# Performance work log

Measured on AMD Instinct MI355X. Metric: run time of the kernel, lower is better.

Reference implementation:

```python
import jax, jax.numpy as jnp
import numpy as np

C = 256
DK = C // 8  # query/key channels


def setup_inputs() -> dict:
    key = jax.random.key(0)
    ks = jax.random.split(key, 7)
    B, W, H = 4, 64, 64
    x = jax.random.normal(ks[0], (B, C, W, H), dtype=jnp.float32)
    s_in = 1.0 / np.sqrt(C)
    Wq = jax.random.normal(ks[1], (DK, C), dtype=jnp.float32) * s_in
    bq = jnp.zeros((DK,), dtype=jnp.float32)
    Wk = jax.random.normal(ks[2], (DK, C), dtype=jnp.float32) * s_in
    bk = jnp.zeros((DK,), dtype=jnp.float32)
    Wv = jax.random.normal(ks[3], (C, C), dtype=jnp.float32) * s_in
    bv = jnp.zeros((C,), dtype=jnp.float32)
    return {"x": x, "Wq": Wq, "bq": bq, "Wk": Wk, "bk": bk, "Wv": Wv, "bv": bv}


def reference(x, Wq, bq, Wk, bk, Wv, bv):
    B, Cc, W, H = x.shape
    N = W * H
    xf = x.reshape(B, Cc, N)  # (B, C, N) flattened spatial
    # 1x1 convs == channel matmuls
    q = jnp.einsum('dc,bcn->bnd', Wq, xf) + bq  # (B, N, DK)
    k = jnp.einsum('dc,bcn->bdn', Wk, xf) + bk[None, :, None]  # (B, DK, N)
    v = jnp.einsum('oc,bcn->bon', Wv, xf) + bv[None, :, None]  # (B, C, N)
    energy = jnp.einsum('bnd,bdm->bnm', q, k) / jnp.sqrt(jnp.float32(q.shape[-1]))
    attn = jax.nn.softmax(energy, axis=-1)  # (B, N, N)
    out = jnp.einsum('bcn,bmn->bcm', v, attn)  # v @ attn^T
    return out.reshape(B, Cc, W, H) + x
```

## Files before the change

kernel.cpp:

```cpp
#include <hip/hip_runtime.h>
#include <hip/hip_bf16.h>
#include <math.h>

#define BB 4
#define CC 256
#define DKK 32
#define NN 4096
#define QSCALE 0.2550181864060454f

typedef __attribute__((ext_vector_type(8))) __bf16 bf16x8;
typedef __attribute__((ext_vector_type(4))) __bf16 bf16x4;
typedef __attribute__((ext_vector_type(4))) float f32x4;

#define XST 260
#define SCRST 65

__global__ __launch_bounds__(256) void qkv_kernel(
    const float* __restrict__ x,
    const float* __restrict__ Wq, const float* __restrict__ bq,
    const float* __restrict__ Wk, const float* __restrict__ bk,
    const float* __restrict__ Wv, const float* __restrict__ bv,
    __bf16* __restrict__ qws, __bf16* __restrict__ kws, __bf16* __restrict__ vws)
{
    __shared__ __align__(16) unsigned char smem[50688];
    __bf16* xsT  = (__bf16*)smem;
    float*  xs32 = (float*)(smem + 33280);
    float*  scr  = (float*)(smem + 33280);

    const int tid = threadIdx.x;
    const int w   = tid >> 6;
    const int l   = tid & 63;
    const int l15 = l & 15;
    const int lq  = l >> 4;
    const int n0  = blockIdx.x * 64;
    const int b   = blockIdx.y;

    for (int cr = 0; cr < 4; cr++) {
#pragma unroll
        for (int p = 0; p < 4; p++) {
            int cc = p * 16 + (tid >> 4);
            int nf = (tid & 15) * 4;
            float4 v = *(const float4*)&x[((size_t)(b * CC + cr * 64 + cc)) * NN + n0 + nf];
            *(float4*)&xs32[cc * 68 + nf] = v;
        }
        __syncthreads();
        {
            int n = tid >> 2, cs = (tid & 3) * 16;
            bf16x4 t0, t1, t2, t3;
#pragma unroll
            for (int j = 0; j < 4; j++) {
                t0[j] = (__bf16)xs32[(cs + j)      * 68 + n];
                t1[j] = (__bf16)xs32[(cs + 4 + j)  * 68 + n];
                t2[j] = (__bf16)xs32[(cs + 8 + j)  * 68 + n];
                t3[j] = (__bf16)xs32[(cs + 12 + j) * 68 + n];
            }
            *(bf16x4*)&xsT[n * XST + cr * 64 + cs]      = t0;
            *(bf16x4*)&xsT[n * XST + cr * 64 + cs + 4]  = t1;
            *(bf16x4*)&xsT[n * XST + cr * 64 + cs + 8]  = t2;
            *(bf16x4*)&xsT[n * XST + cr * 64 + cs + 12] = t3;
        }
        __syncthreads();
    }

    const float* wp[5];
#pragma unroll
    for (int ot = 0; ot < 5; ot++) {
        int ob = 80 * w + 16 * ot;
        const float* src = (ob < 32) ? (Wq + (size_t)ob * CC)
                         : (ob < 64) ? (Wk + (size_t)(ob - 32) * CC)
                                     : (Wv + (size_t)(ob - 64) * CC);
        wp[ot] = src + (size_t)l15 * CC;
    }

    const f32x4 zf = {0.f, 0.f, 0.f, 0.f};
    f32x4 acc[5][4];
#pragma unroll
    for (int i = 0; i < 5; i++)
#pragma unroll
        for (int j = 0; j < 4; j++) acc[i][j] = zf;

    float4 wc[5][2], wn[5][2];
#pragma unroll
    for (int ot = 0; ot < 5; ot++) {
        wc[ot][0] = *(const float4*)(wp[ot] + lq * 8);
        wc[ot][1] = *(const float4*)(wp[ot] + lq * 8 + 4);
    }
#pragma unroll
    for (int ks = 0; ks < 8; ks++) {
        if (ks < 7) {
#pragma unroll
            for (int ot = 0; ot < 5; ot++) {
                wn[ot][0] = *(const float4*)(wp[ot] + (ks + 1) * 32 + lq * 8);
                wn[ot][1] = *(const float4*)(wp[ot] + (ks + 1) * 32 + lq * 8 + 4);
            }
        }
        bf16x8 bfr[4];
#pragma unroll
        for (int nt = 0; nt < 4; nt++) {
            bf16x4 lo = *(const bf16x4*)&xsT[(nt * 16 + l15) * XST + ks * 32 + lq * 8];
            bf16x4 hi = *(const bf16x4*)&xsT[(nt * 16 + l15) * XST + ks * 32 + lq * 8 + 4];
            bfr[nt] = __builtin_shufflevector(lo, hi, 0, 1, 2, 3, 4, 5, 6, 7);
        }
#pragma unroll
        for (int ot = 0; ot < 5; ot++) {
            bf16x8 af;
            af[0] = (__bf16)wc[ot][0].x; af[1] = (__bf16)wc[ot][0].y;
            af[2] = (__bf16)wc[ot][0].z; af[3] = (__bf16)wc[ot][0].w;
            af[4] = (__bf16)wc[ot][1].x; af[5] = (__bf16)wc[ot][1].y;
            af[6] = (__bf16)wc[ot][1].z; af[7] = (__bf16)wc[ot][1].w;
#pragma unroll
            for (int nt = 0; nt < 4; nt++)
                acc[ot][nt] = __builtin_amdgcn_mfma_f32_16x16x32_bf16(af, bfr[nt], acc[ot][nt], 0, 0, 0);
        }
        if (ks < 7) {
#pragma unroll
            for (int ot = 0; ot < 5; ot++) { wc[ot][0] = wn[ot][0]; wc[ot][1] = wn[ot][1]; }
        }
    }

    __syncthreads();
    const size_t vbase = (size_t)b * CC * NN;
#pragma unroll
    for (int ot = 0; ot < 5; ot++) {
        int ob = 80 * w + ot * 16;
#pragma unroll
        for (int nt = 0; nt < 4; nt++) {
#pragma unroll
            for (int r = 0; r < 4; r++) {
                int o = ob + lq * 4 + r;
                int n = nt * 16 + l15;
                float val = acc[ot][nt][r];
                if (ob >= 64) {
                    int c = o - 64;
                    int chunk = (n0 >> 5) + (nt >> 1);
                    vws[vbase + (size_t)chunk * 8192 + (5 * w - 4 + ot) * 512
                        + (lq * 4 + r) * 32 + (nt & 1) * 16 + l15] = (__bf16)(val + bv[c]);
                } else if (ob < 32) {
                    scr[o * SCRST + n] = (val + bq[o]) * QSCALE;
                } else {
                    scr[o * SCRST + n] = val + bk[o - 32];
                }
            }
        }
    }
    __syncthreads();
    {
        int n  = tid >> 2;
        int d0 = (tid & 3) * 8;
        bf16x8 qv, kv;
#pragma unroll
        for (int j = 0; j < 8; j++) {
            qv[j] = (__bf16)scr[(d0 + j) * SCRST + n];
            kv[j] = (__bf16)scr[(32 + d0 + j) * SCRST + n];
        }
        size_t base = ((size_t)b * NN + n0 + n) * DKK + d0;
        *(bf16x8*)&qws[base] = qv;
        *(bf16x8*)&kws[base] = kv;
    }
}

#define PST 36
#define MST 68
#define PWSZ (64 * PST)

__global__ __launch_bounds__(256, 2) void attn_kernel(
    const __bf16* __restrict__ qb, const __bf16* __restrict__ kb,
    const __bf16* __restrict__ vt, const float* __restrict__ x,
    float* __restrict__ out)
{
    __shared__ __align__(16) unsigned char smem[38144];
    __bf16* pw   = (__bf16*)smem + (threadIdx.x >> 6) * 2 * PWSZ;
    float*  Ls   = (float*)(smem + 36864);
    float*  Linv = (float*)(smem + 37888);

    const int tid = threadIdx.x;
    const int w   = tid >> 6;
    const int l   = tid & 63;
    const int l15 = l & 15;
    const int lq  = l >> 4;

    const int beta = blockIdx.x;
    const int b    = (beta >> 1) & 3;
    const int ch   = (beta >> 3) & 1;
    const int mt   = ((beta >> 4) << 1) | (beta & 1);
    const int m0   = mt * 64;

    const __bf16* qbb = qb + (size_t)b * NN * DKK;
    const __bf16* kbb = kb + (size_t)b * NN * DKK;
    const __bf16* vtb = vt + (size_t)b * CC * NN;

    bf16x8 qa[4];
#pragma unroll
    for (int af = 0; af < 4; af++)
        qa[af] = *(const bf16x8*)(qbb + (size_t)(m0 + af * 16 + l15) * DKK + lq * 8);

    const __bf16* kstrip = kbb + (size_t)(w * 32 + l15) * DKK + lq * 8;
    const __bf16* vstrip = vtb + (size_t)w * 8192 + (size_t)ch * 4096
                               + l15 * 32 + lq * 8;

    const f32x4 zf = {0.f, 0.f, 0.f, 0.f};
    f32x4 acc[4][8];
#pragma unroll
    for (int i = 0; i < 4; i++)
#pragma unroll
        for (int j = 0; j < 8; j++) acc[i][j] = zf;
    float lacc[4] = {0.f, 0.f, 0.f, 0.f};

    bf16x8 kA0 = *(const bf16x8*)kstrip;
    bf16x8 kA1 = *(const bf16x8*)(kstrip + 16 * DKK);
#pragma unroll
    for (int af = 0; af < 4; af++) {
        f32x4 e0 = __builtin_amdgcn_mfma_f32_16x16x32_bf16(kA0, qa[af], zf, 0, 0, 0);
        f32x4 e1 = __builtin_amdgcn_mfma_f32_16x16x32_bf16(kA1, qa[af], zf, 0, 0, 0);
        bf16x4 p0, p1;
#pragma unroll
        for (int r = 0; r < 4; r++) {
            float v0 = __builtin_amdgcn_exp2f(e0[r]); lacc[af] += v0; p0[r] = (__bf16)v0;
            float v1 = __builtin_amdgcn_exp2f(e1[r]); lacc[af] += v1; p1[r] = (__bf16)v1;
        }
        *(bf16x4*)&pw[(af * 16 + l15) * PST + lq * 4]      = p0;
        *(bf16x4*)&pw[(af * 16 + l15) * PST + 16 + lq * 4] = p1;
    }
    kA0 = *(const bf16x8*)(kstrip + (size_t)128 * DKK);
    kA1 = *(const bf16x8*)(kstrip + (size_t)144 * DKK);

#pragma unroll 2
    for (int ic = 0; ic < 31; ic++) {
        const int cur = ic & 1;
        const __bf16* vch = vstrip + (size_t)ic * 32768;

        bf16x8 vfC[4], vfN[4];
#pragma unroll
        for (int ct = 0; ct < 4; ct++)
            vfC[ct] = *(const bf16x8*)(vch + ct * 512);

        bf16x8 pf[4];
#pragma unroll
        for (int af = 0; af < 4; af++) {
            bf16x4 plo = *(const bf16x4*)&pw[cur * PWSZ + (af * 16 + l15) * PST + lq * 8];
            bf16x4 phi = *(const bf16x4*)&pw[cur * PWSZ + (af * 16 + l15) * PST + lq * 8 + 4];
            pf[af] = __builtin_shufflevector(plo, phi, 0, 1, 2, 3, 4, 5, 6, 7);
        }

#pragma unroll
        for (int af = 0; af < 4; af++) {
            f32x4 e0 = __builtin_amdgcn_mfma_f32_16x16x32_bf16(kA0, qa[af], zf, 0, 0, 0);
            f32x4 e1 = __builtin_amdgcn_mfma_f32_16x16x32_bf16(kA1, qa[af], zf, 0, 0, 0);
            bf16x4 p0, p1;
#pragma unroll
            for (int r = 0; r < 4; r++) {
                float v0 = __builtin_amdgcn_exp2f(e0[r]); lacc[af] += v0; p0[r] = (__bf16)v0;
                float v1 = __builtin_amdgcn_exp2f(e1[r]); lacc[af] += v1; p1[r] = (__bf16)v1;
            }
            *(bf16x4*)&pw[(cur ^ 1) * PWSZ + (af * 16 + l15) * PST + lq * 4]      = p0;
            *(bf16x4*)&pw[(cur ^ 1) * PWSZ + (af * 16 + l15) * PST + 16 + lq * 4] = p1;
        }
        kA0 = *(const bf16x8*)(kstrip + (size_t)(ic + 2) * 128 * DKK);
        kA1 = *(const bf16x8*)(kstrip + (size_t)((ic + 2) * 128 + 16) * DKK);

#pragma unroll
        for (int ct = 0; ct < 4; ct++)
            vfN[ct] = *(const bf16x8*)(vch + (4 + ct) * 512);
#pragma unroll
        for (int ct = 0; ct < 4; ct++)
#pragma unroll
            for (int af = 0; af < 4; af++)
                acc[af][ct] = __builtin_amdgcn_mfma_f32_16x16x32_bf16(vfC[ct], pf[af], acc[af][ct], 0, 0, 0);
#pragma unroll
        for (int ct = 0; ct < 4; ct++)
#pragma unroll
            for (int af = 0; af < 4; af++)
                acc[af][4 + ct] = __builtin_amdgcn_mfma_f32_16x16x32_bf16(vfN[ct], pf[af], acc[af][4 + ct], 0, 0, 0);
    }

    {
        const __bf16* vch = vstrip + (size_t)31 * 32768;
        bf16x8 pf[4];
#pragma unroll
        for (int af = 0; af < 4; af++) {
            bf16x4 plo = *(const bf16x4*)&pw[(31 & 1) * PWSZ + (af * 16 + l15) * PST + lq * 8];
            bf16x4 phi = *(const bf16x4*)&pw[(31 & 1) * PWSZ + (af * 16 + l15) * PST + lq * 8 + 4];
            pf[af] = __builtin_shufflevector(plo, phi, 0, 1, 2, 3, 4, 5, 6, 7);
        }
        bf16x8 vfC[4], vfN[4];
#pragma unroll
        for (int ct = 0; ct < 4; ct++) vfC[ct] = *(const bf16x8*)(vch + ct * 512);
#pragma unroll
        for (int ct = 0; ct < 4; ct++) vfN[ct] = *(const bf16x8*)(vch + (4 + ct) * 512);
#pragma unroll
        for (int ct = 0; ct < 4; ct++)
#pragma unroll
            for (int af = 0; af < 4; af++)
                acc[af][ct] = __builtin_amdgcn_mfma_f32_16x16x32_bf16(vfC[ct], pf[af], acc[af][ct], 0, 0, 0);
#pragma unroll
        for (int ct = 0; ct < 4; ct++)
#pragma unroll
            for (int af = 0; af < 4; af++)
                acc[af][4 + ct] = __builtin_amdgcn_mfma_f32_16x16x32_bf16(vfN[ct], pf[af], acc[af][4 + ct], 0, 0, 0);
    }

#pragma unroll
    for (int af = 0; af < 4; af++) {
        lacc[af] += __shfl_xor(lacc[af], 16, 64);
        lacc[af] += __shfl_xor(lacc[af], 32, 64);
    }
    if (lq == 0) {
#pragma unroll
        for (int af = 0; af < 4; af++) Ls[w * 64 + af * 16 + l15] = lacc[af];
    }
    __syncthreads();
    if (tid < 64)
        Linv[tid] = 1.0f / (Ls[tid] + Ls[64 + tid] + Ls[128 + tid] + Ls[192 + tid]);

    float* Ored = (float*)smem + w * (32 * MST);
#pragma unroll
    for (int q = 0; q < 4; q++) {
        if (q > 0) __syncthreads();
#pragma unroll
        for (int ctp = 0; ctp < 2; ctp++) {
            int ct = 2 * q + ctp;
#pragma unroll
            for (int af = 0; af < 4; af++) {
#pragma unroll
                for (int r = 0; r < 4; r++)
                    Ored[(ctp * 16 + lq * 4 + r) * MST + af * 16 + l15] = acc[af][ct][r];
            }
        }
        __syncthreads();
        const int cl  = tid >> 3;
        const int mi0 = (tid & 7) * 8;
        const float* Ob = (const float*)smem + cl * MST;
#pragma unroll
        for (int j = 0; j < 2; j++) {
            int mi = mi0 + 4 * j;
            f32x4 s = *(const f32x4*)&Ob[mi];
            s = s + *(const f32x4*)&Ob[1 * (32 * MST) + mi];
            s = s + *(const f32x4*)&Ob[2 * (32 * MST) + mi];
            s = s + *(const f32x4*)&Ob[3 * (32 * MST) + mi];
            f32x4 li = *(const f32x4*)&Linv[mi];
            int c = ch * 128 + q * 32 + cl;
            size_t gi = ((size_t)(b * CC + c)) * NN + m0 + mi;
            f32x4 xr = *(const f32x4*)&x[gi];
            *(f32x4*)&out[gi] = s * li + xr;
        }
    }
}

extern "C" void kernel_launch(void* const* d_in, const int* in_sizes, int n_in,
                              void* d_out, int out_size, void* d_ws, size_t ws_size,
                              hipStream_t stream) {
    const float* x  = (const float*)d_in[0];
    const float* Wq = (const float*)d_in[1];
    const float* bq = (const float*)d_in[2];
    const float* Wk = (const float*)d_in[3];
    const float* bk = (const float*)d_in[4];
    const float* Wv = (const float*)d_in[5];
    const float* bv = (const float*)d_in[6];
    float* out = (float*)d_out;

    __bf16* qws = (__bf16*)d_ws;
    __bf16* kws = qws + (size_t)BB * NN * DKK;
    __bf16* vws = kws + (size_t)BB * NN * DKK;

    qkv_kernel<<<dim3(64, BB), 256, 0, stream>>>(x, Wq, bq, Wk, bk, Wv, bv,
                                                 qws, kws, vws);
    attn_kernel<<<dim3(512), 256, 0, stream>>>(qws, kws, vws, x, out);
}
```

Before: 157.4 us.

## Halve QKV projection tile to 32 columns and load x directly into transposed LDS

```diff
diff --git a/kernel.cpp b/kernel.cpp
--- a/kernel.cpp
+++ b/kernel.cpp
@@ -13,53 +13,40 @@
 typedef __attribute__((ext_vector_type(4))) float f32x4;
 
 #define XST 260
-#define SCRST 65
-
-__global__ __launch_bounds__(256) void qkv_kernel(
+#define SCRST 33
+
+__global__ __launch_bounds__(256, 2) void qkv_kernel(
     const float* __restrict__ x,
     const float* __restrict__ Wq, const float* __restrict__ bq,
     const float* __restrict__ Wk, const float* __restrict__ bk,
     const float* __restrict__ Wv, const float* __restrict__ bv,
     __bf16* __restrict__ qws, __bf16* __restrict__ kws, __bf16* __restrict__ vws)
 {
-    __shared__ __align__(16) unsigned char smem[50688];
-    __bf16* xsT  = (__bf16*)smem;
-    float*  xs32 = (float*)(smem + 33280);
-    float*  scr  = (float*)(smem + 33280);
+    __shared__ __align__(16) unsigned char smem[16640];
+    __bf16* xsT = (__bf16*)smem;
+    float*  scr = (float*)smem;
 
     const int tid = threadIdx.x;
     const int w   = tid >> 6;
     const int l   = tid & 63;
     const int l15 = l & 15;
     const int lq  = l >> 4;
-    const int n0  = blockIdx.x * 64;
+    const int n0  = blockIdx.x * 32;
     const int b   = blockIdx.y;
 
-    for (int cr = 0; cr < 4; cr++) {
-#pragma unroll
-        for (int p = 0; p < 4; p++) {
-            int cc = p * 16 + (tid >> 4);
-            int nf = (tid & 15) * 4;
-            float4 v = *(const float4*)&x[((size_t)(b * CC + cr * 64 + cc)) * NN + n0 + nf];
-            *(float4*)&xs32[cc * 68 + nf] = v;
-        }
-        __syncthreads();
-        {
-            int n = tid >> 2, cs = (tid & 3) * 16;
-            bf16x4 t0, t1, t2, t3;
-#pragma unroll
-            for (int j = 0; j < 4; j++) {
-                t0[j] = (__bf16)xs32[(cs + j)      * 68 + n];
-                t1[j] = (__bf16)xs32[(cs + 4 + j)  * 68 + n];
-                t2[j] = (__bf16)xs32[(cs + 8 + j)  * 68 + n];
-                t3[j] = (__bf16)xs32[(cs + 12 + j) * 68 + n];
-            }
-            *(bf16x4*)&xsT[n * XST + cr * 64 + cs]      = t0;
-            *(bf16x4*)&xsT[n * XST + cr * 64 + cs + 4]  = t1;
-            *(bf16x4*)&xsT[n * XST + cr * 64 + cs + 8]  = t2;
-            *(bf16x4*)&xsT[n * XST + cr * 64 + cs + 12] = t3;
-        }
-        __syncthreads();
+    {
+        const int cb = tid >> 3;
+        const int nf = (tid & 7) * 4;
+        const float* xp = x + ((size_t)(b * CC) + cb) * NN + n0 + nf;
+#pragma unroll
+        for (int r = 0; r < 8; r++) {
+            float4 v = *(const float4*)(xp + (size_t)r * 32 * NN);
+            int c = r * 32 + cb;
+            xsT[(nf + 0) * XST + c] = (__bf16)v.x;
+            xsT[(nf + 1) * XST + c] = (__bf16)v.y;
+            xsT[(nf + 2) * XST + c] = (__bf16)v.z;
+            xsT[(nf + 3) * XST + c] = (__bf16)v.w;
+        }
     }
 
     const float* wp[5];
@@ -72,19 +59,22 @@
         wp[ot] = src + (size_t)l15 * CC;
     }
 
-    const f32x4 zf = {0.f, 0.f, 0.f, 0.f};
-    f32x4 acc[5][4];
-#pragma unroll
-    for (int i = 0; i < 5; i++)
-#pragma unroll
-        for (int j = 0; j < 4; j++) acc[i][j] = zf;
-
     float4 wc[5][2], wn[5][2];
 #pragma unroll
     for (int ot = 0; ot < 5; ot++) {
         wc[ot][0] = *(const float4*)(wp[ot] + lq * 8);
         wc[ot][1] = *(const float4*)(wp[ot] + lq * 8 + 4);
     }
+
+    __syncthreads();
+
+    const f32x4 zf = {0.f, 0.f, 0.f, 0.f};
+    f32x4 acc[5][2];
+#pragma unroll
+    for (int i = 0; i < 5; i++)
+#pragma unroll
+        for (int j = 0; j < 2; j++) acc[i][j] = zf;
+
 #pragma unroll
     for (int ks = 0; ks < 8; ks++) {
         if (ks < 7) {
@@ -94,9 +84,9 @@
                 wn[ot][1] = *(const float4*)(wp[ot] + (ks + 1) * 32 + lq * 8 + 4);
             }
         }
-        bf16x8 bfr[4];
-#pragma unroll
-        for (int nt = 0; nt < 4; nt++) {
+        bf16x8 bfr[2];
+#pragma unroll
+        for (int nt = 0; nt < 2; nt++) {
             bf16x4 lo = *(const bf16x4*)&xsT[(nt * 16 + l15) * XST + ks * 32 + lq * 8];
             bf16x4 hi = *(const bf16x4*)&xsT[(nt * 16 + l15) * XST + ks * 32 + lq * 8 + 4];
             bfr[nt] = __builtin_shufflevector(lo, hi, 0, 1, 2, 3, 4, 5, 6, 7);
@@ -109,7 +99,7 @@
             af[4] = (__bf16)wc[ot][1].x; af[5] = (__bf16)wc[ot][1].y;
             af[6] = (__bf16)wc[ot][1].z; af[7] = (__bf16)wc[ot][1].w;
 #pragma unroll
-            for (int nt = 0; nt < 4; nt++)
+            for (int nt = 0; nt < 2; nt++)
                 acc[ot][nt] = __builtin_amdgcn_mfma_f32_16x16x32_bf16(af, bfr[nt], acc[ot][nt], 0, 0, 0);
         }
         if (ks < 7) {
@@ -119,12 +109,13 @@
     }
 
     __syncthreads();
-    const size_t vbase = (size_t)b * CC * NN;
+
+    __bf16* vchunk = vws + (size_t)b * CC * NN + (size_t)(n0 >> 5) * 8192;
 #pragma unroll
     for (int ot = 0; ot < 5; ot++) {
         int ob = 80 * w + ot * 16;
 #pragma unroll
-        for (int nt = 0; nt < 4; nt++) {
+        for (int nt = 0; nt < 2; nt++) {
 #pragma unroll
             for (int r = 0; r < 4; r++) {
                 int o = ob + lq * 4 + r;
@@ -132,9 +123,8 @@
                 float val = acc[ot][nt][r];
                 if (ob >= 64) {
                     int c = o - 64;
-                    int chunk = (n0 >> 5) + (nt >> 1);
-                    vws[vbase + (size_t)chunk * 8192 + (5 * w - 4 + ot) * 512
-                        + (lq * 4 + r) * 32 + (nt & 1) * 16 + l15] = (__bf16)(val + bv[c]);
+                    vchunk[(5 * w - 4 + ot) * 512 + (lq * 4 + r) * 32 + n] =
+                        (__bf16)(val + bv[c]);
                 } else if (ob < 32) {
                     scr[o * SCRST + n] = (val + bq[o]) * QSCALE;
                 } else {
@@ -145,17 +135,17 @@
     }
     __syncthreads();
     {
-        int n  = tid >> 2;
-        int d0 = (tid & 3) * 8;
-        bf16x8 qv, kv;
-#pragma unroll
-        for (int j = 0; j < 8; j++) {
+        int n  = tid >> 3;
+        int d0 = (tid & 7) * 4;
+        bf16x4 qv, kv;
+#pragma unroll
+        for (int j = 0; j < 4; j++) {
             qv[j] = (__bf16)scr[(d0 + j) * SCRST + n];
             kv[j] = (__bf16)scr[(32 + d0 + j) * SCRST + n];
         }
         size_t base = ((size_t)b * NN + n0 + n) * DKK + d0;
-        *(bf16x8*)&qws[base] = qv;
-        *(bf16x8*)&kws[base] = kv;
+        *(bf16x4*)&qws[base] = qv;
+        *(bf16x4*)&kws[base] = kv;
     }
 }
 
@@ -362,7 +352,7 @@
     __bf16* kws = qws + (size_t)BB * NN * DKK;
     __bf16* vws = kws + (size_t)BB * NN * DKK;
 
-    qkv_kernel<<<dim3(64, BB), 256, 0, stream>>>(x, Wq, bq, Wk, bk, Wv, bv,
-                                                 qws, kws, vws);
+    qkv_kernel<<<dim3(128, BB), 256, 0, stream>>>(x, Wq, bq, Wk, bk, Wv, bv,
+                                                  qws, kws, vws);
     attn_kernel<<<dim3(512), 256, 0, stream>>>(qws, kws, vws, x, out);
 }
```

New measurement: 153.1 us. 2.8% less time.
